# Kernel tuning notes

Hardware: AMD Instinct MI355X
Metric: run time of the kernel (lower is better)

## Reference

```python
import jax, jax.numpy as jnp
import numpy as np

B, F, CTX, HID, L, NB = 16384, 64, 128, 512, 8, 2


def setup_inputs() -> dict:
    key = jax.random.key(0)
    ks = jax.random.split(key, 8)
    inputs = jax.random.normal(ks[0], (B, F), jnp.float32)
    context = jax.random.normal(ks[1], (B, CTX), jnp.float32)
    n_id = F // 2                      # identity features per coupling layer
    in_dim = n_id + CTX                # coupling net input = identity half + context
    out_dim = F                        # 2 * num_transform_features (shift | scale)
    s_in = 1.0 / np.sqrt(in_dim)
    s_h = 1.0 / np.sqrt(HID)
    W_in = jax.random.uniform(ks[2], (L, in_dim, HID), jnp.float32, -s_in, s_in)
    b_in = jax.random.uniform(ks[3], (L, HID), jnp.float32, -s_in, s_in)
    W_h = jax.random.uniform(ks[4], (L, NB, HID, HID), jnp.float32, -s_h, s_h)
    b_h = jax.random.uniform(ks[5], (L, NB, HID), jnp.float32, -s_h, s_h)
    # output layer init: normal(0, 0.01) weight, zero bias (as in torch source)
    W_out = 0.01 * jax.random.normal(ks[6], (L, HID, out_dim), jnp.float32)
    b_out = jnp.zeros((L, out_dim), jnp.float32)
    # fixed random permutations between coupling layers (nflows RandomPermutation buffers)
    rng = np.random.RandomState(42)
    perms = jnp.asarray(np.stack([rng.permutation(F) for _ in range(L - 1)]), jnp.int32)
    return dict(inputs=inputs, context=context, W_in=W_in, b_in=b_in,
                W_h=W_h, b_h=b_h, W_out=W_out, b_out=b_out, perms=perms)


def reference(inputs, context, W_in, b_in, W_h, b_h, W_out, b_out, perms):
    F_ = inputs.shape[-1]
    n_layers = W_in.shape[0]
    n_blocks = W_h.shape[1]
    nt = F_ // 2  # num transform features
    even_idx = jnp.arange(0, F_, 2)
    odd_idx = jnp.arange(1, F_, 2)
    x = jnp.clip(inputs, -1.0, 1.0)
    logdet = jnp.zeros(x.shape[0], x.dtype)
    for i in range(n_layers):
        # mask[::2]=1 for even layers -> mask>0 (even indices) are TRANSFORM features
        if i % 2 == 0:
            t_idx, id_idx = even_idx, odd_idx
        else:
            t_idx, id_idx = odd_idx, even_idx
        id_split = x[:, id_idx]   # [B, nt]
        tr_split = x[:, t_idx]    # [B, nt]
        h = jax.nn.relu(jnp.concatenate([id_split, context], -1) @ W_in[i] + b_in[i])
        for j in range(n_blocks):
            h = jax.nn.relu(h @ W_h[i, j] + b_h[i, j])
        p = h @ W_out[i] + b_out[i]            # [B, 2*nt]
        shift = p[:, :nt]
        scale = jax.nn.sigmoid(p[:, nt:] + 2.0) + 1e-3
        logdet = logdet + jnp.sum(jnp.log(scale), axis=-1)
        x = x.at[:, t_idx].set(tr_split * scale + shift).at[:, id_idx].set(id_split)
        if i < n_layers - 1:
            x = x[:, perms[i]]
    return jnp.clip(x, -1.0, 1.0), logdet
```

## Files before the change

### kernel.cpp

```cpp
#include <hip/hip_runtime.h>


typedef float v4f  __attribute__((ext_vector_type(4)));
typedef float v16f __attribute__((ext_vector_type(16)));
typedef int   v4i  __attribute__((ext_vector_type(4)));
typedef int   v8i  __attribute__((ext_vector_type(8)));
typedef unsigned char uchar;
typedef unsigned long long ull;

#define BATCH 16384
#define NF    64
#define NCTX  128
#define NL    8

#define RS     528
#define HHALF  256
#define AST    208
#define AHALF  96

#define WSCALE     16.0f
#define WSCALE_INV 0.0625f

#define WIN_EPL   (192 * 512)
#define WH_EPB    (512 * 512)
#define WOUT_EPL  (512 * 64)
#define OFF_WIN   ((size_t)0)
#define OFF_WH    ((size_t)(8 * WIN_EPL))
#define OFF_WOUT  (OFF_WH + (size_t)(16 * WH_EPB))
#define TOT_PACK_ELEMS (OFF_WOUT + (size_t)(8 * WOUT_EPL))
#define NEED_WS   (TOT_PACK_ELEMS)

#define NU_IN   192
#define NU_H    1024
#define NU_OUT  128
#define NU_TOT  (NU_IN + NU_H + NU_OUT)

template<bool HI>
__device__ __forceinline__ unsigned int pk2(float a, float b, unsigned int old) {
    return __builtin_amdgcn_cvt_pk_fp8_f32(a, b, old, HI);
}
__device__ __forceinline__ uchar q8(float v) {
    return (uchar)(__builtin_amdgcn_cvt_pk_fp8_f32(v, v, 0u, false) & 0xffu);
}

__device__ __forceinline__ void bar_lds() {
    asm volatile("s_waitcnt lgkmcnt(0)" ::: "memory");
    __builtin_amdgcn_s_barrier();
    asm volatile("" ::: "memory");
}

__global__ __launch_bounds__(256) void pack_weights_kernel(
    const float* __restrict__ W_in,
    const float* __restrict__ W_h,
    const float* __restrict__ W_out,
    unsigned char* __restrict__ ws) {
    const int wid  = (blockIdx.x * blockDim.x + threadIdx.x) >> 6;
    const int lane = threadIdx.x & 63;
    if (wid >= NU_TOT) return;

    if (wid < NU_IN + NU_H) {
        const float* src;
        uchar* dstbase;
        int kb, khalf, g, rawK;
        if (wid < NU_IN) {
            int i = wid / 24, r = wid % 24;
            kb = r >> 3; khalf = (r >> 2) & 1; g = r & 3;
            src = W_in + (size_t)i * (160 * 512); rawK = 160;
            dstbase = ws + OFF_WIN + (size_t)i * WIN_EPL + kb * 32768;
        } else {
            int u = wid - NU_IN;
            int ij = u >> 6, r = u & 63;
            kb = r >> 3; khalf = (r >> 2) & 1; g = r & 3;
            src = W_h + (size_t)ij * WH_EPB; rawK = 512;
            dstbase = ws + OFF_WH + (size_t)ij * WH_EPB + kb * 32768;
        }
        const int pig = (g == 1) ? 2 : (g == 2) ? 1 : g;
        const int k0  = kb * 64 + khalf * 32 + pig * 8;
        const int n0  = lane * 8;
        float v[8][8];
        if (k0 < rawK) {
#pragma unroll
            for (int j = 0; j < 8; ++j) {
                const float* p = src + (size_t)(k0 + j) * 512 + n0;
                float4 a = ((const float4*)p)[0];
                float4 b = ((const float4*)p)[1];
                v[j][0] = a.x * WSCALE; v[j][1] = a.y * WSCALE;
                v[j][2] = a.z * WSCALE; v[j][3] = a.w * WSCALE;
                v[j][4] = b.x * WSCALE; v[j][5] = b.y * WSCALE;
                v[j][6] = b.z * WSCALE; v[j][7] = b.w * WSCALE;
            }
        } else {
#pragma unroll
            for (int j = 0; j < 8; ++j)
#pragma unroll
                for (int nn = 0; nn < 8; ++nn) v[j][nn] = 0.f;
        }
        uchar* dst = dstbase +
            ((lane >> 2) * 64 + 32 * khalf + (lane & 3) * 8) * 32 + g * 8;
#pragma unroll
        for (int nn = 0; nn < 8; ++nn) {
            uint2 o;
            o.x = pk2<false>(v[0][nn], v[1][nn], 0u);
            o.x = pk2<true >(v[2][nn], v[3][nn], o.x);
            o.y = pk2<false>(v[4][nn], v[5][nn], 0u);
            o.y = pk2<true >(v[6][nn], v[7][nn], o.y);
            *(uint2*)(dst + nn * 32) = o;
        }
    } else {
        int u = wid - (NU_IN + NU_H);
        int i = u >> 4, kc = u & 15;
        const int n = lane;
        const float* src = W_out + (size_t)i * WOUT_EPL;
        float v[32];
#pragma unroll
        for (int k = 0; k < 32; ++k)
            v[k] = src[(size_t)(kc * 32 + k) * 64 + n] * WSCALE;
        uchar* dst = ws + OFF_WOUT + (size_t)i * 32768 +
                     (size_t)(kc >> 2) * 8192 + (size_t)(n >> 4) * 2048 +
                     (size_t)((((kc & 3) << 4) | (n & 15)) * 32);
        const int pig_tab[4] = {0, 2, 1, 3};
#pragma unroll
        for (int g = 0; g < 4; ++g) {
            const int kk0 = pig_tab[g] * 8;
            uint2 o;
            o.x = pk2<false>(v[kk0 + 0], v[kk0 + 1], 0u);
            o.x = pk2<true >(v[kk0 + 2], v[kk0 + 3], o.x);
            o.y = pk2<false>(v[kk0 + 4], v[kk0 + 5], 0u);
            o.y = pk2<true >(v[kk0 + 6], v[kk0 + 7], o.y);
            *(uint2*)(dst + g * 8) = o;
        }
    }
}

__device__ __forceinline__ v16f mfma32(ull a, ull b, v16f c) {
    return __builtin_amdgcn_mfma_f32_32x32x16_fp8_fp8((long)a, (long)b, c, 0, 0, 0);
}
__device__ __forceinline__ v4f mfma16(ull a, ull b, v4f c) {
    return __builtin_amdgcn_mfma_f32_16x16x32_fp8_fp8((long)a, (long)b, c, 0, 0, 0);
}
__device__ __forceinline__ v16f mfma64(v8i a, v8i b, v16f c) {
    return __builtin_amdgcn_mfma_scale_f32_32x32x64_f8f6f4(
        a, b, c, 0, 0, 0, 0x7f7f7f7f, 0, 0x7f7f7f7f);
}
__device__ __forceinline__ v4f mfma128(v8i a, v8i b, v4f c) {
    return __builtin_amdgcn_mfma_scale_f32_16x16x128_f8f6f4(
        a, b, c, 0, 0, 0, 0x7f7f7f7f, 0, 0x7f7f7f7f);
}

__device__ __forceinline__ v8i ldv8(const uchar* p) {
    v4i lo = *(const v4i*)p;
    v4i hi = *(const v4i*)(p + 16);
    return __builtin_shufflevector(lo, hi, 0, 1, 2, 3, 4, 5, 6, 7);
}

struct BPre  { v8i b00, b10, b01, b11; };
struct BPre16 { v8i u0, v0, u1, v1; };

__device__ __forceinline__ BPre prefB(const uchar* __restrict__ wpk,
                                      int pair, int lane) {
    const uchar* bp = wpk + (size_t)(pair * 128 + lane) * 32;
    BPre r;
    r.b00 = ldv8(bp);
    r.b10 = ldv8(bp + 2048);
    r.b01 = ldv8(bp + 32768);
    r.b11 = ldv8(bp + 32768 + 2048);
    return r;
}
__device__ __forceinline__ BPre16 prefB16(const uchar* __restrict__ wpk,
                                          int w, int lane) {
    const int npair = w & 1;
    const uchar* b0 = wpk + (size_t)npair * 2048 + (size_t)lane * 32;
    const uchar* b1 = wpk + (size_t)(npair + 2) * 2048 + (size_t)lane * 32;
    BPre16 r;
    r.u0 = ldv8(b0);        r.v0 = ldv8(b1);
    r.u1 = ldv8(b0 + 8192); r.v1 = ldv8(b1 + 8192);
    return r;
}

template<int NKB>
__device__ __forceinline__ void gemm32mx(
    const uchar* __restrict__ wpk,
    const float* __restrict__ bias,
    const uchar* __restrict__ Abuf, int ast, int halfoff,
    uchar* __restrict__ Obuf,
    int pair, int lane, BPre pre)
{
    const int l31 = lane & 31, hl = lane >> 5;
    v16f a00, a01, a10, a11;
#pragma unroll
    for (int r = 0; r < 16; ++r) { a00[r] = 0.f; a01[r] = 0.f;
                                   a10[r] = 0.f; a11[r] = 0.f; }
    const uchar* aLo0 = Abuf + l31 * ast + hl * 16;
    const uchar* aHi0 = aLo0 + halfoff;
    const uchar* aLo1 = aLo0 + 32 * ast;
    const uchar* aHi1 = aHi0 + 32 * ast;
    const uchar* bp = wpk + (size_t)(pair * 128 + lane) * 32;

    auto loadB = [&](int s, int kb) -> v8i {
        if (kb >= NKB) kb = NKB - 1;
        return ldv8(bp + s * 2048 + (size_t)kb * 32768);
    };
    auto loadA = [&](const uchar* lo_, const uchar* hi_, int kb) -> v8i {
        if (kb >= NKB) kb = NKB - 1;
        v4i lo = *(const v4i*)(lo_ + kb * 32);
        v4i hi = *(const v4i*)(hi_ + kb * 32);
        return __builtin_shufflevector(lo, hi, 0, 1, 2, 3, 4, 5, 6, 7);
    };

    v8i xA0 = loadA(aLo0, aHi0, 0), xA1 = loadA(aLo1, aHi1, 0);
    v8i xB0 = loadA(aLo0, aHi0, 1), xB1 = loadA(aLo1, aHi1, 1);
    v8i b00 = pre.b00, b10 = pre.b10;
    v8i b01 = pre.b01, b11 = pre.b11;
#pragma unroll 1
    for (int kb = 0; kb + 1 < NKB; kb += 2) {
        a00 = mfma64(b00, xA0, a00);
        a01 = mfma64(b00, xA1, a01);
        a10 = mfma64(b10, xA0, a10);
        a11 = mfma64(b10, xA1, a11);
        xA0 = loadA(aLo0, aHi0, kb + 2);
        xA1 = loadA(aLo1, aHi1, kb + 2);
        b00 = loadB(0, kb + 2);
        b10 = loadB(1, kb + 2);
        a00 = mfma64(b01, xB0, a00);
        a01 = mfma64(b01, xB1, a01);
        a10 = mfma64(b11, xB0, a10);
        a11 = mfma64(b11, xB1, a11);
        xB0 = loadA(aLo0, aHi0, kb + 3);
        xB1 = loadA(aLo1, aHi1, kb + 3);
        b01 = loadB(0, kb + 3);
        b11 = loadB(1, kb + 3);
    }
    if constexpr (NKB & 1) {
        a00 = mfma64(b00, xA0, a00);
        a01 = mfma64(b00, xA1, a01);
        a10 = mfma64(b10, xA0, a10);
        a11 = mfma64(b10, xA1, a11);
    }

    const uchar* ob0 = Obuf + l31 * RS + 4 * hl;
    const uchar* ob1 = ob0 + 32 * RS;
    auto emit = [&](const v16f& am0, const v16f& am1, int strip) {
#pragma unroll
        for (int q = 0; q < 4; ++q) {
            const int n0 = strip * 32 + q * 8 + 4 * hl;
            float4 bv = *(const float4*)(bias + n0);
            unsigned int u0, u1;
            u0 = pk2<false>(fmaxf(fmaf(am0[4 * q + 0], WSCALE_INV, bv.x), 0.f),
                            fmaxf(fmaf(am0[4 * q + 1], WSCALE_INV, bv.y), 0.f), 0u);
            u0 = pk2<true >(fmaxf(fmaf(am0[4 * q + 2], WSCALE_INV, bv.z), 0.f),
                            fmaxf(fmaf(am0[4 * q + 3], WSCALE_INV, bv.w), 0.f), u0);
            u1 = pk2<false>(fmaxf(fmaf(am1[4 * q + 0], WSCALE_INV, bv.x), 0.f),
                            fmaxf(fmaf(am1[4 * q + 1], WSCALE_INV, bv.y), 0.f), 0u);
            u1 = pk2<true >(fmaxf(fmaf(am1[4 * q + 2], WSCALE_INV, bv.z), 0.f),
                            fmaxf(fmaf(am1[4 * q + 3], WSCALE_INV, bv.w), 0.f), u1);
            const int g = strip * 4 + q;
            const int off = (g & 1) * HHALF + ((g >> 1) << 3);
            *(unsigned int*)(ob0 + off) = u0;
            *(unsigned int*)(ob1 + off) = u1;
        }
    };
    emit(a00, a01, pair * 2 + 0);
    emit(a10, a11, pair * 2 + 1);
}

template<int KC>
__device__ __forceinline__ void gemm32_raw(
    const float* __restrict__ wraw,
    const float* __restrict__ bias,
    const uchar* __restrict__ Abuf, int ast, int ahalf,
    uchar* __restrict__ Obuf,
    int strip, int lane)
{
    constexpr int P = KC / 2;
    const int l31 = lane & 31, hl = lane >> 5;
    v16f acc0, acc1;
#pragma unroll
    for (int r = 0; r < 16; ++r) { acc0[r] = 0.f; acc1[r] = 0.f; }
    const uchar* a0p = Abuf + l31 * ast + hl * ahalf;
    const uchar* a1p = a0p + 32 * ast;

    auto loadB = [&](int kc) -> ull {
        if (kc >= KC) kc = KC - 1;
        int n  = strip * 32 + l31;
        int k0 = kc * 16 + hl * 8;
        unsigned int lo, hi;
        lo = pk2<false>(wraw[(size_t)(k0 + 0) * 512 + n] * WSCALE,
                        wraw[(size_t)(k0 + 1) * 512 + n] * WSCALE, 0u);
        lo = pk2<true >(wraw[(size_t)(k0 + 2) * 512 + n] * WSCALE,
                        wraw[(size_t)(k0 + 3) * 512 + n] * WSCALE, lo);
        hi = pk2<false>(wraw[(size_t)(k0 + 4) * 512 + n] * WSCALE,
                        wraw[(size_t)(k0 + 5) * 512 + n] * WSCALE, 0u);
        hi = pk2<true >(wraw[(size_t)(k0 + 6) * 512 + n] * WSCALE,
                        wraw[(size_t)(k0 + 7) * 512 + n] * WSCALE, hi);
        return ((ull)hi << 32) | (ull)lo;
    };

    ull b0 = loadB(0), b1 = loadB(1), b2 = loadB(2), b3 = loadB(3);
    int p2 = 0;
#pragma unroll 1
    for (; p2 + 1 < P; p2 += 2) {
        ulonglong2 Aa0 = *(const ulonglong2*)(a0p + p2 * 16);
        ulonglong2 Aa1 = *(const ulonglong2*)(a1p + p2 * 16);
        acc0 = mfma32(Aa0.x, b0, acc0);
        acc1 = mfma32(Aa1.x, b0, acc1);
        b0 = loadB(2 * p2 + 4);
        acc0 = mfma32(Aa0.y, b1, acc0);
        acc1 = mfma32(Aa1.y, b1, acc1);
        b1 = loadB(2 * p2 + 5);
        ulonglong2 Ab0 = *(const ulonglong2*)(a0p + p2 * 16 + 16);
        ulonglong2 Ab1 = *(const ulonglong2*)(a1p + p2 * 16 + 16);
        acc0 = mfma32(Ab0.x, b2, acc0);
        acc1 = mfma32(Ab1.x, b2, acc1);
        b2 = loadB(2 * p2 + 6);
        acc0 = mfma32(Ab0.y, b3, acc0);
        acc1 = mfma32(Ab1.y, b3, acc1);
        b3 = loadB(2 * p2 + 7);
    }
    if constexpr (P & 1) {
        ulonglong2 Aa0 = *(const ulonglong2*)(a0p + (P - 1) * 16);
        ulonglong2 Aa1 = *(const ulonglong2*)(a1p + (P - 1) * 16);
        acc0 = mfma32(Aa0.x, b0, acc0);
        acc1 = mfma32(Aa1.x, b0, acc1);
        acc0 = mfma32(Aa0.y, b1, acc0);
        acc1 = mfma32(Aa1.y, b1, acc1);
    }

    const int n = strip * 32 + l31;
    const int nb = ((n >> 3) & 1) * HHALF + ((n >> 4) << 3) + (n & 7);
    const float bv = bias[n];
#pragma unroll
    for (int reg = 0; reg < 16; ++reg) {
        int row = (reg & 3) + 8 * (reg >> 2) + 4 * hl;
        float v0 = fmaxf(fmaf(acc0[reg], WSCALE_INV, bv), 0.f);
        Obuf[row * RS + nb] = q8(v0);
        float v1 = fmaxf(fmaf(acc1[reg], WSCALE_INV, bv), 0.f);
        Obuf[(row + 32) * RS + nb] = q8(v1);
    }
}

template<bool PACKED>
__device__ __forceinline__ float gemm16_fused(
    const uchar* __restrict__ wpk,
    const float* __restrict__ wraw,
    const float* __restrict__ bias,
    const uchar* __restrict__ Abuf,
    float* __restrict__ xbuf,
    const int* __restrict__ ct,
    int par, int w, int lane, BPre16 pre)
{
    const int quad = lane >> 4, l15 = lane & 15;
    const int mtb  = w >> 1;
    const int npair = w & 1;
    const int ntb0 = npair, ntb1 = npair + 2;
    const int row  = mtb * 16 + l15;
    v4f acc0, acc1;
    acc0[0] = acc0[1] = acc0[2] = acc0[3] = 0.f;
    acc1[0] = acc1[1] = acc1[2] = acc1[3] = 0.f;

    if constexpr (PACKED) {
        const uchar* ab = Abuf + row * RS + quad * 16;
        auto loadX = [&](int kb) -> v8i {
            const uchar* p = ab + kb * 64;
            v4i lo = *(const v4i*)p;
            v4i hi = *(const v4i*)(p + HHALF);
            return __builtin_shufflevector(lo, hi, 0, 1, 2, 3, 4, 5, 6, 7);
        };
        const uchar* bw0 = wpk + (size_t)ntb0 * 2048 + (size_t)lane * 32;
        const uchar* bw1 = wpk + (size_t)ntb1 * 2048 + (size_t)lane * 32;

        v8i x0 = loadX(0);
        v8i u0 = pre.u0, v0 = pre.v0;
        v8i u1 = pre.u1, v1 = pre.v1;
        acc0 = mfma128(u0, x0, acc0);
        acc1 = mfma128(v0, x0, acc1);
        v8i x1 = loadX(1);
        u0 = ldv8(bw0 + 2 * 8192); v0 = ldv8(bw1 + 2 * 8192);
        acc0 = mfma128(u1, x1, acc0);
        acc1 = mfma128(v1, x1, acc1);
        x0 = loadX(2);
        u1 = ldv8(bw0 + 3 * 8192); v1 = ldv8(bw1 + 3 * 8192);
        acc0 = mfma128(u0, x0, acc0);
        acc1 = mfma128(v0, x0, acc1);
        x1 = loadX(3);
        acc0 = mfma128(u1, x1, acc0);
        acc1 = mfma128(v1, x1, acc1);
    } else {
        const uchar* ap = Abuf + row * RS + (quad & 1) * HHALF + ((quad >> 1) << 3);
        constexpr int KC = 16;
        auto loadB = [&](int ntb, int kc) -> ull {
            if (kc >= KC) kc = KC - 1;
            int n  = ntb * 16 + l15;
            int k0 = kc * 32 + quad * 8;
            unsigned int lo, hi;
            lo = pk2<false>(wraw[(size_t)(k0 + 0) * 64 + n] * WSCALE,
                            wraw[(size_t)(k0 + 1) * 64 + n] * WSCALE, 0u);
            lo = pk2<true >(wraw[(size_t)(k0 + 2) * 64 + n] * WSCALE,
                            wraw[(size_t)(k0 + 3) * 64 + n] * WSCALE, lo);
            hi = pk2<false>(wraw[(size_t)(k0 + 4) * 64 + n] * WSCALE,
                            wraw[(size_t)(k0 + 5) * 64 + n] * WSCALE, 0u);
            hi = pk2<true >(wraw[(size_t)(k0 + 6) * 64 + n] * WSCALE,
                            wraw[(size_t)(k0 + 7) * 64 + n] * WSCALE, hi);
            return ((ull)hi << 32) | (ull)lo;
        };
        auto rdA = [&](int kc) -> ull {
            if (kc >= KC) kc = KC - 1;
            return *(const ull*)(ap + kc * 16);
        };
        ull a0 = rdA(0), a1 = rdA(1), a2 = rdA(2), a3 = rdA(3);
        ull u0 = loadB(ntb0, 0), u1 = loadB(ntb0, 1);
        ull u2 = loadB(ntb0, 2), u3 = loadB(ntb0, 3);
        ull v0 = loadB(ntb1, 0), v1 = loadB(ntb1, 1);
        ull v2 = loadB(ntb1, 2), v3 = loadB(ntb1, 3);
        int kc = 0;
#pragma unroll 1
        for (; kc + 3 < KC; kc += 4) {
            acc0 = mfma16(u0, a0, acc0); acc1 = mfma16(v0, a0, acc1);
            a0 = rdA(kc + 4);
            u0 = loadB(ntb0, kc + 4); v0 = loadB(ntb1, kc + 4);
            acc0 = mfma16(u1, a1, acc0); acc1 = mfma16(v1, a1, acc1);
            a1 = rdA(kc + 5);
            u1 = loadB(ntb0, kc + 5); v1 = loadB(ntb1, kc + 5);
            acc0 = mfma16(u2, a2, acc0); acc1 = mfma16(v2, a2, acc1);
            a2 = rdA(kc + 6);
            u2 = loadB(ntb0, kc + 6); v2 = loadB(ntb1, kc + 6);
            acc0 = mfma16(u3, a3, acc0); acc1 = mfma16(v3, a3, acc1);
            a3 = rdA(kc + 7);
            u3 = loadB(ntb0, kc + 7); v3 = loadB(ntb1, kc + 7);
        }
    }

    const int n0 = ntb0 * 16 + quad * 4;
    float ld = 0.f;
#pragma unroll
    for (int r = 0; r < 4; ++r) {
        float shiftv = fmaf(acc0[r], WSCALE_INV, bias[n0 + r]);
        float z      = fmaf(acc1[r], WSCALE_INV, bias[32 + n0 + r]) + 2.0f;
        float s      = 1.0f / (1.0f + __expf(-z)) + 0.001f;
        int sc = n0 + r;
        int tc = ct[2 * sc + par];
        float xo = xbuf[row * NF + tc];
        xbuf[row * NF + tc] = xo * s + shiftv;
        ld += __logf(s);
    }
    return ld;
}

template<bool PACKED>
__global__ __launch_bounds__(512, 2) void flow_kernel(
    const float* __restrict__ inputs,
    const float* __restrict__ ctx,
    const float* __restrict__ W_in,  const float* __restrict__ b_in,
    const float* __restrict__ W_h,   const float* __restrict__ b_h,
    const float* __restrict__ W_out, const float* __restrict__ b_out,
    const int*   __restrict__ perms,
    const uchar* __restrict__ wpk,
    float* __restrict__ out)
{
    __shared__ __align__(16) uchar hbuf0[64 * RS];
    __shared__ __align__(16) uchar hbuf1[64 * RS];
    __shared__ __align__(16) uchar abuf[64 * AST];
    __shared__ __align__(16) float xbuf[64 * NF];
    __shared__ int Ctab[NL * NF];

    const int tid  = threadIdx.x;
    const int wave = tid >> 6;
    const int lane = tid & 63;
    const int trow = tid >> 3;
    const int t8   = tid & 7;
    const int row0 = blockIdx.x * 64;

    {
        int i = tid >> 6, c = tid & 63;
        int idx = c;
        for (int k = i - 1; k >= 0; --k) idx = perms[k * NF + idx];
        Ctab[tid] = idx;
    }
    {
#pragma unroll
        for (int j = 0; j < 2; ++j) {
            float4 v = ((const float4*)(inputs + (size_t)row0 * NF))[tid + j * 512];
            v.x = fminf(fmaxf(v.x, -1.f), 1.f);
            v.y = fminf(fmaxf(v.y, -1.f), 1.f);
            v.z = fminf(fmaxf(v.z, -1.f), 1.f);
            v.w = fminf(fmaxf(v.w, -1.f), 1.f);
            ((float4*)xbuf)[tid + j * 512] = v;
        }
    }
    {
        const float* crow = ctx + (size_t)(row0 + trow) * NCTX + t8 * 16;
        float4 f0 = ((const float4*)crow)[0];
        float4 f1 = ((const float4*)crow)[1];
        float4 f2 = ((const float4*)crow)[2];
        float4 f3 = ((const float4*)crow)[3];
        uint2 ck0, ck1;
        ck0.x = pk2<false>(f0.x, f0.y, 0u);
        ck0.x = pk2<true >(f0.z, f0.w, ck0.x);
        ck0.y = pk2<false>(f1.x, f1.y, 0u);
        ck0.y = pk2<true >(f1.z, f1.w, ck0.y);
        ck1.x = pk2<false>(f2.x, f2.y, 0u);
        ck1.x = pk2<true >(f2.z, f2.w, ck1.x);
        ck1.y = pk2<false>(f3.x, f3.y, 0u);
        ck1.y = pk2<true >(f3.z, f3.w, ck1.y);
        *(uint2*)(abuf + trow * AST + (2 + t8) * 8) = ck0;
        *(uint2*)(abuf + trow * AST + AHALF + (2 + t8) * 8) = ck1;
    }
    if (tid < 256) {
        int r = tid >> 2, q = tid & 3;
        *(ull*)(abuf + r * AST + (q & 1) * AHALF + 80 + ((q >> 1) << 3)) = 0ULL;
    }
    float ld_acc = 0.f;

    BPre preN;
    if constexpr (PACKED) preN = prefB(wpk + OFF_WIN, wave, lane);
    bar_lds();

#pragma unroll 1
    for (int i = 0; i < NL; ++i) {
        const int par = i & 1;
        const int idp = par ^ 1;
        const int* ct = Ctab + i * NF;

        if (t8 < 4) {
            const float* xr = xbuf + trow * NF;
            uint2 idv;
            idv.x = pk2<false>(xr[ct[2 * (t8 * 8 + 0) + idp]],
                               xr[ct[2 * (t8 * 8 + 1) + idp]], 0u);
            idv.x = pk2<true >(xr[ct[2 * (t8 * 8 + 2) + idp]],
                               xr[ct[2 * (t8 * 8 + 3) + idp]], idv.x);
            idv.y = pk2<false>(xr[ct[2 * (t8 * 8 + 4) + idp]],
                               xr[ct[2 * (t8 * 8 + 5) + idp]], 0u);
            idv.y = pk2<true >(xr[ct[2 * (t8 * 8 + 6) + idp]],
                               xr[ct[2 * (t8 * 8 + 7) + idp]], idv.y);
            *(uint2*)(abuf + trow * AST + (t8 & 1) * AHALF + ((t8 >> 1) << 3)) = idv;
        }
        bar_lds();

        if constexpr (PACKED) {
            const uchar* wg1 = wpk + OFF_WH + (size_t)(i * 2 + 0) * WH_EPB;
            const uchar* wg2 = wpk + OFF_WH + (size_t)(i * 2 + 1) * WH_EPB;
            const uchar* wg3 = wpk + OFF_WOUT + (size_t)i * 32768;
            gemm32mx<3>(wpk + OFF_WIN + (size_t)i * WIN_EPL, b_in + i * 512,
                        abuf, AST, AHALF, hbuf0, wave, lane, preN);
            BPre pre1 = prefB(wg1, wave, lane);
            bar_lds();
            gemm32mx<8>(wg1, b_h + (i * 2 + 0) * 512,
                        hbuf0, RS, HHALF, hbuf1, wave, lane, pre1);
            BPre pre2 = prefB(wg2, wave, lane);
            bar_lds();
            gemm32mx<8>(wg2, b_h + (i * 2 + 1) * 512,
                        hbuf1, RS, HHALF, hbuf0, wave, lane, pre2);
            BPre16 pre3 = prefB16(wg3, wave, lane);
            bar_lds();
            ld_acc += gemm16_fused<true>(
                wg3, W_out + (size_t)i * WOUT_EPL, b_out + i * 64,
                hbuf0, xbuf, ct, par, wave, lane, pre3);
            preN = prefB(wpk + OFF_WIN + (size_t)((i + 1) & 7) * WIN_EPL,
                         wave, lane);
            bar_lds();
        } else {
            gemm32_raw<10>(W_in + (size_t)i * (160 * 512), b_in + i * 512,
                           abuf, AST, AHALF, hbuf0, wave * 2 + 0, lane);
            gemm32_raw<10>(W_in + (size_t)i * (160 * 512), b_in + i * 512,
                           abuf, AST, AHALF, hbuf0, wave * 2 + 1, lane);
            bar_lds();
            gemm32_raw<32>(W_h + (size_t)(i * 2 + 0) * WH_EPB,
                           b_h + (i * 2 + 0) * 512,
                           hbuf0, RS, HHALF, hbuf1, wave * 2 + 0, lane);
            gemm32_raw<32>(W_h + (size_t)(i * 2 + 0) * WH_EPB,
                           b_h + (i * 2 + 0) * 512,
                           hbuf0, RS, HHALF, hbuf1, wave * 2 + 1, lane);
            bar_lds();
            gemm32_raw<32>(W_h + (size_t)(i * 2 + 1) * WH_EPB,
                           b_h + (i * 2 + 1) * 512,
                           hbuf1, RS, HHALF, hbuf0, wave * 2 + 0, lane);
            gemm32_raw<32>(W_h + (size_t)(i * 2 + 1) * WH_EPB,
                           b_h + (i * 2 + 1) * 512,
                           hbuf1, RS, HHALF, hbuf0, wave * 2 + 1, lane);
            bar_lds();
            BPre16 dummy{};
            ld_acc += gemm16_fused<false>(
                (const uchar*)0, W_out + (size_t)i * WOUT_EPL, b_out + i * 64,
                hbuf0, xbuf, ct, par, wave, lane, dummy);
            bar_lds();
        }
    }

    {
        const int* c7 = Ctab + 7 * NF;
#pragma unroll
        for (int j = 0; j < 2; ++j) {
            int p = tid + j * 512;
            int r = p >> 4, c0 = (p & 15) * 4;
            const float* xr = xbuf + r * NF;
            float4 v;
            v.x = fminf(fmaxf(xr[c7[c0 + 0]], -1.f), 1.f);
            v.y = fminf(fmaxf(xr[c7[c0 + 1]], -1.f), 1.f);
            v.z = fminf(fmaxf(xr[c7[c0 + 2]], -1.f), 1.f);
            v.w = fminf(fmaxf(xr[c7[c0 + 3]], -1.f), 1.f);
            ((float4*)(out + (size_t)row0 * NF))[p] = v;
        }
    }
    {
        float* lbuf = (float*)abuf;
        const int rrow = (wave >> 1) * 16 + (lane & 15);
        const int slot = (wave & 1) * 4 + (lane >> 4);
        lbuf[rrow * 8 + slot] = ld_acc;
        bar_lds();
        if (tid < 64) {
            float s = 0.f;
#pragma unroll
            for (int k = 0; k < 8; ++k) s += lbuf[tid * 8 + k];
            out[(size_t)BATCH * NF + row0 + tid] = s;
        }
    }
}

extern "C" void kernel_launch(void* const* d_in, const int* in_sizes, int n_in,
                              void* d_out, int out_size, void* d_ws, size_t ws_size,
                              hipStream_t stream) {
    const float* inputs  = (const float*)d_in[0];
    const float* context = (const float*)d_in[1];
    const float* W_in    = (const float*)d_in[2];
    const float* b_in    = (const float*)d_in[3];
    const float* W_h     = (const float*)d_in[4];
    const float* b_h     = (const float*)d_in[5];
    const float* W_out   = (const float*)d_in[6];
    const float* b_out   = (const float*)d_in[7];
    const int*   perms   = (const int*)d_in[8];
    float* out = (float*)d_out;

    if (ws_size >= (size_t)NEED_WS) {
        uchar* ws = (uchar*)d_ws;
        const int total_threads = NU_TOT * 64;
        pack_weights_kernel<<<(total_threads + 255) / 256, 256, 0, stream>>>(
            W_in, W_h, W_out, ws);
        flow_kernel<true><<<256, 512, 0, stream>>>(
            inputs, context, W_in, b_in, W_h, b_h, W_out, b_out, perms, ws, out);
    } else {
        flow_kernel<false><<<256, 512, 0, stream>>>(
            inputs, context, W_in, b_in, W_h, b_h, W_out, b_out, perms,
            (const uchar*)0, out);
    }
}
```

Before: 185.6 us.

## Re-permute FP8 K ordering so GEMM epilogue writes 16-byte LDS stores

```diff
diff --git a/kernel.cpp b/kernel.cpp
--- a/kernel.cpp
+++ b/kernel.cpp
@@ -47,6 +47,10 @@
     asm volatile("s_waitcnt lgkmcnt(0)" ::: "memory");
     __builtin_amdgcn_s_barrier();
     asm volatile("" ::: "memory");
+}
+
+__device__ __forceinline__ int kqg(int g) {
+    return (g & 1) * 16 + ((g >> 1) & 1) * 4;
 }
 
 __global__ __launch_bounds__(256) void pack_weights_kernel(
@@ -74,14 +78,15 @@
             src = W_h + (size_t)ij * WH_EPB; rawK = 512;
             dstbase = ws + OFF_WH + (size_t)ij * WH_EPB + kb * 32768;
         }
-        const int pig = (g == 1) ? 2 : (g == 2) ? 1 : g;
-        const int k0  = kb * 64 + khalf * 32 + pig * 8;
-        const int n0  = lane * 8;
+        const int kbase = kb * 64 + khalf * 32;
+        const int kq    = kqg(g);
+        const int n0    = lane * 8;
         float v[8][8];
-        if (k0 < rawK) {
+        if (kbase < rawK) {
 #pragma unroll
             for (int j = 0; j < 8; ++j) {
-                const float* p = src + (size_t)(k0 + j) * 512 + n0;
+                const int kj = kbase + kq + (j >> 2) * 8 + (j & 3);
+                const float* p = src + (size_t)kj * 512 + n0;
                 float4 a = ((const float4*)p)[0];
                 float4 b = ((const float4*)p)[1];
                 v[j][0] = a.x * WSCALE; v[j][1] = a.y * WSCALE;
@@ -118,15 +123,14 @@
         uchar* dst = ws + OFF_WOUT + (size_t)i * 32768 +
                      (size_t)(kc >> 2) * 8192 + (size_t)(n >> 4) * 2048 +
                      (size_t)((((kc & 3) << 4) | (n & 15)) * 32);
-        const int pig_tab[4] = {0, 2, 1, 3};
 #pragma unroll
         for (int g = 0; g < 4; ++g) {
-            const int kk0 = pig_tab[g] * 8;
+            const int kq = kqg(g);
             uint2 o;
-            o.x = pk2<false>(v[kk0 + 0], v[kk0 + 1], 0u);
-            o.x = pk2<true >(v[kk0 + 2], v[kk0 + 3], o.x);
-            o.y = pk2<false>(v[kk0 + 4], v[kk0 + 5], 0u);
-            o.y = pk2<true >(v[kk0 + 6], v[kk0 + 7], o.y);
+            o.x = pk2<false>(v[kq + 0], v[kq + 1], 0u);
+            o.x = pk2<true >(v[kq + 2], v[kq + 3], o.x);
+            o.y = pk2<false>(v[kq + 8], v[kq + 9], 0u);
+            o.y = pk2<true >(v[kq + 10], v[kq + 11], o.y);
             *(uint2*)(dst + g * 8) = o;
         }
     }
@@ -237,9 +241,10 @@
         a11 = mfma64(b10, xA1, a11);
     }
 
-    const uchar* ob0 = Obuf + l31 * RS + 4 * hl;
+    const uchar* ob0 = Obuf + l31 * RS + hl * HHALF;
     const uchar* ob1 = ob0 + 32 * RS;
     auto emit = [&](const v16f& am0, const v16f& am1, int strip) {
+        v4i w0, w1;
 #pragma unroll
         for (int q = 0; q < 4; ++q) {
             const int n0 = strip * 32 + q * 8 + 4 * hl;
@@ -253,11 +258,11 @@
                             fmaxf(fmaf(am1[4 * q + 1], WSCALE_INV, bv.y), 0.f), 0u);
             u1 = pk2<true >(fmaxf(fmaf(am1[4 * q + 2], WSCALE_INV, bv.z), 0.f),
                             fmaxf(fmaf(am1[4 * q + 3], WSCALE_INV, bv.w), 0.f), u1);
-            const int g = strip * 4 + q;
-            const int off = (g & 1) * HHALF + ((g >> 1) << 3);
-            *(unsigned int*)(ob0 + off) = u0;
-            *(unsigned int*)(ob1 + off) = u1;
-        }
+            w0[q] = (int)u0;
+            w1[q] = (int)u1;
+        }
+        *(v4i*)(ob0 + strip * 16) = w0;
+        *(v4i*)(ob1 + strip * 16) = w1;
     };
     emit(a00, a01, pair * 2 + 0);
     emit(a10, a11, pair * 2 + 1);
@@ -492,21 +497,44 @@
         float4 f1 = ((const float4*)crow)[1];
         float4 f2 = ((const float4*)crow)[2];
         float4 f3 = ((const float4*)crow)[3];
-        uint2 ck0, ck1;
-        ck0.x = pk2<false>(f0.x, f0.y, 0u);
-        ck0.x = pk2<true >(f0.z, f0.w, ck0.x);
-        ck0.y = pk2<false>(f1.x, f1.y, 0u);
-        ck0.y = pk2<true >(f1.z, f1.w, ck0.y);
-        ck1.x = pk2<false>(f2.x, f2.y, 0u);
-        ck1.x = pk2<true >(f2.z, f2.w, ck1.x);
-        ck1.y = pk2<false>(f3.x, f3.y, 0u);
-        ck1.y = pk2<true >(f3.z, f3.w, ck1.y);
-        *(uint2*)(abuf + trow * AST + (2 + t8) * 8) = ck0;
-        *(uint2*)(abuf + trow * AST + AHALF + (2 + t8) * 8) = ck1;
-    }
-    if (tid < 256) {
-        int r = tid >> 2, q = tid & 3;
-        *(ull*)(abuf + r * AST + (q & 1) * AHALF + 80 + ((q >> 1) << 3)) = 0ULL;
+        if constexpr (PACKED) {
+            const int B0 = (1 + (t8 >> 1)) * 16 + (t8 & 1) * 8;
+            uint2 r0, r1;
+            r0.x = pk2<false>(f0.x, f0.y, 0u);
+            r0.x = pk2<true >(f0.z, f0.w, r0.x);
+            r0.y = pk2<false>(f2.x, f2.y, 0u);
+            r0.y = pk2<true >(f2.z, f2.w, r0.y);
+            r1.x = pk2<false>(f1.x, f1.y, 0u);
+            r1.x = pk2<true >(f1.z, f1.w, r1.x);
+            r1.y = pk2<false>(f3.x, f3.y, 0u);
+            r1.y = pk2<true >(f3.z, f3.w, r1.y);
+            *(uint2*)(abuf + trow * AST + B0) = r0;
+            *(uint2*)(abuf + trow * AST + AHALF + B0) = r1;
+        } else {
+            uint2 ck0, ck1;
+            ck0.x = pk2<false>(f0.x, f0.y, 0u);
+            ck0.x = pk2<true >(f0.z, f0.w, ck0.x);
+            ck0.y = pk2<false>(f1.x, f1.y, 0u);
+            ck0.y = pk2<true >(f1.z, f1.w, ck0.y);
+            ck1.x = pk2<false>(f2.x, f2.y, 0u);
+            ck1.x = pk2<true >(f2.z, f2.w, ck1.x);
+            ck1.y = pk2<false>(f3.x, f3.y, 0u);
+            ck1.y = pk2<true >(f3.z, f3.w, ck1.y);
+            *(uint2*)(abuf + trow * AST + (2 + t8) * 8) = ck0;
+            *(uint2*)(abuf + trow * AST + AHALF + (2 + t8) * 8) = ck1;
+        }
+    }
+    if constexpr (PACKED) {
+        if (tid < 128) {
+            int r = tid >> 1, reg = tid & 1;
+            v4i z; z[0] = z[1] = z[2] = z[3] = 0;
+            *(v4i*)(abuf + r * AST + reg * AHALF + 80) = z;
+        }
+    } else {
+        if (tid < 256) {
+            int r = tid >> 2, q = tid & 3;
+            *(ull*)(abuf + r * AST + (q & 1) * AHALF + 80 + ((q >> 1) << 3)) = 0ULL;
+        }
     }
     float ld_acc = 0.f;
 
@@ -522,16 +550,30 @@
 
         if (t8 < 4) {
             const float* xr = xbuf + trow * NF;
-            uint2 idv;
-            idv.x = pk2<false>(xr[ct[2 * (t8 * 8 + 0) + idp]],
-                               xr[ct[2 * (t8 * 8 + 1) + idp]], 0u);
-            idv.x = pk2<true >(xr[ct[2 * (t8 * 8 + 2) + idp]],
-                               xr[ct[2 * (t8 * 8 + 3) + idp]], idv.x);
-            idv.y = pk2<false>(xr[ct[2 * (t8 * 8 + 4) + idp]],
-                               xr[ct[2 * (t8 * 8 + 5) + idp]], 0u);
-            idv.y = pk2<true >(xr[ct[2 * (t8 * 8 + 6) + idp]],
-                               xr[ct[2 * (t8 * 8 + 7) + idp]], idv.y);
-            *(uint2*)(abuf + trow * AST + (t8 & 1) * AHALF + ((t8 >> 1) << 3)) = idv;
+            if constexpr (PACKED) {
+                unsigned int r0, r1;
+                r0 = pk2<false>(xr[ct[2 * (t8 * 8 + 0) + idp]],
+                                xr[ct[2 * (t8 * 8 + 1) + idp]], 0u);
+                r0 = pk2<true >(xr[ct[2 * (t8 * 8 + 2) + idp]],
+                                xr[ct[2 * (t8 * 8 + 3) + idp]], r0);
+                r1 = pk2<false>(xr[ct[2 * (t8 * 8 + 4) + idp]],
+                                xr[ct[2 * (t8 * 8 + 5) + idp]], 0u);
+                r1 = pk2<true >(xr[ct[2 * (t8 * 8 + 6) + idp]],
+                                xr[ct[2 * (t8 * 8 + 7) + idp]], r1);
+                *(unsigned int*)(abuf + trow * AST + t8 * 4) = r0;
+                *(unsigned int*)(abuf + trow * AST + AHALF + t8 * 4) = r1;
+            } else {
+                uint2 idv;
+                idv.x = pk2<false>(xr[ct[2 * (t8 * 8 + 0) + idp]],
+                                   xr[ct[2 * (t8 * 8 + 1) + idp]], 0u);
+                idv.x = pk2<true >(xr[ct[2 * (t8 * 8 + 2) + idp]],
+                                   xr[ct[2 * (t8 * 8 + 3) + idp]], idv.x);
+                idv.y = pk2<false>(xr[ct[2 * (t8 * 8 + 4) + idp]],
+                                   xr[ct[2 * (t8 * 8 + 5) + idp]], 0u);
+                idv.y = pk2<true >(xr[ct[2 * (t8 * 8 + 6) + idp]],
+                                   xr[ct[2 * (t8 * 8 + 7) + idp]], idv.y);
+                *(uint2*)(abuf + trow * AST + (t8 & 1) * AHALF + ((t8 >> 1) << 3)) = idv;
+            }
         }
         bar_lds();
 
```

Measured after the change: 181.8 us, median of 2. 1.02x faster.
